# Optimization experiments

Measured on AMD Instinct MI355X. Metric: run time of the kernel, lower is better.

## Reference

```python
import jax, jax.numpy as jnp
import numpy as np

NUM_CLASSES = 2
THRESH = 0.5        # overlap_thresh
NEGPOS = 3          # neg:pos ratio
VAR = (0.1, 0.2)    # cfg['variance']
B, P, O = 64, 32768, 50


def point_form(p):
    # center-size [cx,cy,w,h] -> corner [xmin,ymin,xmax,ymax]
    return jnp.concatenate([p[:, :2] - p[:, 2:] * 0.5, p[:, :2] + p[:, 2:] * 0.5], axis=1)


def iou(a, b):
    # a [O,4], b [P,4] corner form -> [O,P]
    lt = jnp.maximum(a[:, None, :2], b[None, :, :2])
    rb = jnp.minimum(a[:, None, 2:], b[None, :, 2:])
    wh = jnp.clip(rb - lt, 0.0, None)
    inter = wh[..., 0] * wh[..., 1]
    area_a = ((a[:, 2] - a[:, 0]) * (a[:, 3] - a[:, 1]))[:, None]
    area_b = ((b[:, 2] - b[:, 0]) * (b[:, 3] - b[:, 1]))[None, :]
    return inter / (area_a + area_b - inter)


def encode(matched, priors_cs):
    g_cxcy = ((matched[:, :2] + matched[:, 2:]) * 0.5 - priors_cs[:, :2]) / (VAR[0] * priors_cs[:, 2:])
    g_wh = jnp.log((matched[:, 2:] - matched[:, :2]) / priors_cs[:, 2:]) / VAR[1]
    return jnp.concatenate([g_cxcy, g_wh], axis=1)


def match_one(truths, labels, priors_cs, priors_pt):
    ovl = iou(truths, priors_pt)                # [O,P]
    best_prior_idx = jnp.argmax(ovl, axis=1)    # [O] best prior per GT
    best_truth_ovl = jnp.max(ovl, axis=0)       # [P]
    best_truth_idx = jnp.argmax(ovl, axis=0)    # [P]
    best_truth_ovl = best_truth_ovl.at[best_prior_idx].set(2.0)
    best_truth_idx = best_truth_idx.at[best_prior_idx].set(jnp.arange(truths.shape[0]))
    matched = truths[best_truth_idx]            # [P,4]
    conf = jnp.where(best_truth_ovl < THRESH, 0, labels[best_truth_idx])
    return encode(matched, priors_cs), conf


def reference(arm_loc, arm_conf, odm_loc, odm_conf, priors, targets):
    loc_data, conf_data = arm_loc, arm_conf    # use_ARM=False -> ARM branch
    num, num_priors = loc_data.shape[0], loc_data.shape[1]
    truths = targets[..., :4]
    labels = (targets[..., 4] >= 0).astype(jnp.int32)   # num_classes == 2 binarization
    priors_pt = point_form(priors)
    loc_t, conf_t = jax.vmap(lambda t, l: match_one(t, l, priors, priors_pt))(truths, labels)
    loc_t = jax.lax.stop_gradient(loc_t)
    conf_t = jax.lax.stop_gradient(conf_t)
    pos = conf_t > 0                             # [B,P]
    # localization: smooth L1, summed over positives
    d = loc_data - loc_t
    ad = jnp.abs(d)
    sl1 = jnp.where(ad < 1.0, 0.5 * d * d, ad - 0.5)
    loss_l = jnp.sum(sl1 * pos[..., None].astype(loc_data.dtype))
    # per-prior conf loss for hard negative mining
    lse = jax.nn.logsumexp(conf_data, axis=-1)   # [B,P]
    picked = jnp.take_along_axis(conf_data, conf_t[..., None], axis=-1)[..., 0]
    lc = lse - picked                            # NLL per prior
    lc_mine = jnp.where(pos, 0.0, lc)            # zero positives before ranking
    order = jnp.argsort(-lc_mine, axis=1)        # descending sort
    rank = jnp.argsort(order, axis=1)            # rank of each prior
    num_pos = jnp.sum(pos, axis=1, keepdims=True)            # [B,1]
    num_neg = jnp.minimum(NEGPOS * num_pos, num_priors - 1)
    neg = rank < num_neg
    sel = (pos | neg).astype(conf_data.dtype)
    loss_c = jnp.sum(lc * sel)
    N = jnp.sum(num_pos).astype(loc_data.dtype)
    return loss_l / N, loss_c / N


def setup_inputs():
    key = jax.random.key(0)
    ks = jax.random.split(key, 8)
    arm_loc = jax.random.normal(ks[0], (B, P, 4), jnp.float32)
    arm_conf = jax.random.normal(ks[1], (B, P, NUM_CLASSES), jnp.float32)
    odm_loc = jax.random.normal(ks[2], (B, P, 4), jnp.float32)
    odm_conf = jax.random.normal(ks[3], (B, P, NUM_CLASSES), jnp.float32)
    # priors in center-size form
    p_cxcy = jax.random.uniform(ks[4], (P, 2), jnp.float32, 0.05, 0.95)
    p_wh = jax.random.uniform(ks[5], (P, 2), jnp.float32, 0.05, 0.5)
    priors = jnp.concatenate([p_cxcy, p_wh], axis=1)
    # GT boxes in corner form with valid extents, labels >= 0
    t_cxcy = jax.random.uniform(ks[6], (B, O, 2), jnp.float32, 0.2, 0.8)
    t_wh = jax.random.uniform(ks[7], (B, O, 2), jnp.float32, 0.05, 0.3)
    boxes = jnp.concatenate([t_cxcy - t_wh * 0.5, t_cxcy + t_wh * 0.5], axis=-1)
    targets = jnp.concatenate([boxes, jnp.ones((B, O, 1), jnp.float32)], axis=-1)
    return {"arm_loc": arm_loc, "arm_conf": arm_conf, "odm_loc": odm_loc,
            "odm_conf": odm_conf, "priors": priors, "targets": targets}
```

## Files before the change

kernel.cpp:

```cpp
#include <hip/hip_runtime.h>
#include <cstdint>

#pragma clang fp contract(off)

#define BB 64
#define PP 32768
#define OO 50
#define THRESH_F 0.5f
#define VAR0 0.1f
#define VAR1 0.2f
#define NEGPOS_I 3
#define SS 32
#define T1 4
#define NB0 2048
#define NB12 1024
#define NCELL 1024

typedef unsigned long long u64;

__device__ __forceinline__ unsigned mpart4(unsigned x) {
    x = (x | (x << 2)) & 0x33u;
    x = (x | (x << 1)) & 0x55u;
    return x;
}
__device__ __forceinline__ int cell_of(float4 pr) {
    int xb = (int)(pr.x * 16.0f); xb = xb < 0 ? 0 : (xb > 15 ? 15 : xb);
    int yb = (int)(pr.y * 16.0f); yb = yb < 0 ? 0 : (yb > 15 ? 15 : yb);
    float s = fmaxf(pr.z, pr.w);
    int wc = s < 0.275f ? 0 : (s < 0.368f ? 1 : (s < 0.44f ? 2 : 3));
    return wc * 256 + (int)(mpart4((unsigned)xb) | (mpart4((unsigned)yb) << 1));
}

__global__ void k_zero(float4* __restrict__ dst, int n4) {
    int i = blockIdx.x * blockDim.x + threadIdx.x;
    if (i < n4) dst[i] = make_float4(0.f, 0.f, 0.f, 0.f);
}

__global__ void k_phist(const float4* __restrict__ pri, int* __restrict__ cnt) {
    int p = blockIdx.x * 1024 + threadIdx.x * 4;
    for (int j = 0; j < 4; ++j)
        atomicAdd(&cnt[cell_of(pri[p + j])], 1);
}

__global__ void k_pscan(const int* __restrict__ cnt, int* __restrict__ base) {
    __shared__ int sc[256];
    int tid = threadIdx.x;
    int a[4]; int s = 0;
    for (int i = 0; i < 4; ++i) { a[i] = cnt[tid * 4 + i]; s += a[i]; }
    sc[tid] = s; __syncthreads();
    for (int off = 1; off < 256; off <<= 1) {
        int v = (tid >= off) ? sc[tid - off] : 0;
        __syncthreads(); sc[tid] += v; __syncthreads();
    }
    int excl = sc[tid] - s;
    for (int i = 0; i < 4; ++i) { base[tid * 4 + i] = excl; excl += a[i]; }
}

__global__ void k_pscat(const float4* __restrict__ pri, const int* __restrict__ base,
                        int* __restrict__ cursor, int* __restrict__ perm) {
    int p = blockIdx.x * 1024 + threadIdx.x * 4;
    for (int j = 0; j < 4; ++j) {
        int c = cell_of(pri[p + j]);
        int pos = base[c] + atomicAdd(&cursor[c], 1);
        perm[pos] = p + j;
    }
}

#define DPP_MAX(x, ctrl, rmask)                                              \
    {                                                                        \
        int _o = __float_as_int(x);                                          \
        x = fmaxf(x, __int_as_float(__builtin_amdgcn_update_dpp(             \
                _o, _o, (ctrl), (rmask), 0xf, false)));                      \
    }
#define DPP_MINI(x, ctrl, rmask)                                             \
    {                                                                        \
        int _o = (x);                                                        \
        int _s = __builtin_amdgcn_update_dpp(_o, _o, (ctrl), (rmask), 0xf, false); \
        x = (_s < x) ? _s : x;                                               \
    }

__device__ __forceinline__ float sl1enc(const float* __restrict__ tb,
                                        float4 pr, float4 ld) {
    float gx = ((tb[0] + tb[2]) * 0.5f - pr.x) / (VAR0 * pr.z);
    float gy = ((tb[1] + tb[3]) * 0.5f - pr.y) / (VAR0 * pr.w);
    float gw = logf((tb[2] - tb[0]) / pr.z) / VAR1;
    float gh = logf((tb[3] - tb[1]) / pr.w) / VAR1;
    float g[4] = {gx, gy, gw, gh};
    float l[4] = {ld.x, ld.y, ld.z, ld.w};
    float s = 0.f;
    for (int q = 0; q < 4; ++q) {
        float d = l[q] - g[q];
        float ad = fabsf(d);
        s += (ad < 1.0f) ? 0.5f * d * d : ad - 0.5f;
    }
    return s;
}

__global__ void __launch_bounds__(256, 8)
k_ml(const float* __restrict__ priors, const int* __restrict__ perm,
     const float* __restrict__ targets,
     const float* __restrict__ arm_loc, const float* __restrict__ arm_conf,
     float* __restrict__ lcm, unsigned char* __restrict__ bpi,
     u64* __restrict__ bpm,
     float* __restrict__ pll, float* __restrict__ pplc, int* __restrict__ pnp,
     int* __restrict__ Hc0, float* __restrict__ Hs0) {
    __shared__ float tr4[OO * 4];
    __shared__ float trA[OO];
    __shared__ int   trL[OO];
    __shared__ int   hc[NB0];
    __shared__ float hs[NB0];
    int b = (blockIdx.x % 8) * 8 + (blockIdx.y % 8);
    int s = (blockIdx.x / 8) + 4 * (blockIdx.y / 8);
    int tid = threadIdx.x;
    for (int i = tid; i < OO * 4; i += 256)
        tr4[i] = targets[(size_t)(b * OO + (i >> 2)) * 5 + (i & 3)];
    if (tid < OO)
        trL[tid] = (targets[(size_t)(b * OO + tid) * 5 + 4] >= 0.0f) ? 1 : 0;
    for (int i = tid; i < NB0; i += 256) { hc[i] = 0; hs[i] = 0.f; }
    __syncthreads();
    if (tid < OO)
        trA[tid] = (tr4[tid*4+2] - tr4[tid*4]) * (tr4[tid*4+3] - tr4[tid*4+1]);
    __syncthreads();

    int p0 = s * (256 * T1) + tid * T1;
    int4 o4 = ((const int4*)perm)[p0 >> 2];
    int o_[T1] = {o4.x, o4.y, o4.z, o4.w};
    int omin = min(min(o_[0], o_[1]), min(o_[2], o_[3]));
    float bx0[T1], by0[T1], bx1[T1], by1[T1], aB[T1];
#pragma unroll
    for (int j = 0; j < T1; ++j) {
        float4 pr = ((const float4*)priors)[o_[j]];
        bx0[j] = pr.x - pr.z * 0.5f; by0[j] = pr.y - pr.w * 0.5f;
        bx1[j] = pr.x + pr.z * 0.5f; by1[j] = pr.y + pr.w * 0.5f;
        aB[j] = (bx1[j] - bx0[j]) * (by1[j] - by0[j]);
    }
    float rbv[T1]; int rbi[T1];
#pragma unroll
    for (int j = 0; j < T1; ++j) { rbv[j] = 0.0f; rbi[j] = 0; }

    for (int t = 0; t < OO; ++t) {
        float t0 = tr4[t*4], t1v = tr4[t*4+1], t2 = tr4[t*4+2], t3 = tr4[t*4+3];
        float aA = trA[t];
        float I[T1];
#pragma unroll
        for (int j = 0; j < T1; ++j) {
            float ltx = fmaxf(t0, bx0[j]), lty = fmaxf(t1v, by0[j]);
            float rbx = fminf(t2, bx1[j]), rby = fminf(t3, by1[j]);
            float wx = fmaxf(rbx - ltx, 0.f), wy = fmaxf(rby - lty, 0.f);
            I[j] = wx * wy;
        }
        bool anyl = (I[0] > 0.f) | (I[1] > 0.f) | (I[2] > 0.f) | (I[3] > 0.f);
        if (__any(anyl)) {
            float cbv = 0.0f; int cbo = omin;
#pragma unroll
            for (int j = 0; j < T1; ++j) {
                float v = I[j] / (aA + aB[j] - I[j]);
                if (v > rbv[j]) { rbv[j] = v; rbi[j] = t; }
                if (v > cbv || (v == cbv && o_[j] < cbo)) { cbv = v; cbo = o_[j]; }
            }
            float x = cbv;
            DPP_MAX(x, 0x111, 0xf);
            DPP_MAX(x, 0x112, 0xf);
            DPP_MAX(x, 0x114, 0xf);
            DPP_MAX(x, 0x118, 0xf);
            DPP_MAX(x, 0x142, 0xa);
            DPP_MAX(x, 0x143, 0xc);
            float mvf = __int_as_float(__builtin_amdgcn_readlane(__float_as_int(x), 63));
            if (mvf > 0.0f) {
                int key = (cbv == mvf) ? cbo : 0x7FFFFFFF;
                DPP_MINI(key, 0x111, 0xf);
                DPP_MINI(key, 0x112, 0xf);
                DPP_MINI(key, 0x114, 0xf);
                DPP_MINI(key, 0x118, 0xf);
                DPP_MINI(key, 0x142, 0xa);
                DPP_MINI(key, 0x143, 0xc);
                int morig = __builtin_amdgcn_readlane(key, 63);
                if ((tid & 63) == 0) {
                    u64 pk = ((u64)__float_as_uint(mvf) << 32) | (unsigned)(PP - morig);
                    atomicMax(&bpm[b * OO + t], pk);
                }
            }
        }
    }

    size_t bbase = (size_t)b * PP;
    float ll = 0.0f, plc = 0.0f; int np = 0;
#pragma unroll
    for (int c = 0; c < T1; ++c) {
        int o = o_[c]; size_t bo = bbase + o;
        int ti = rbi[c]; float ov = rbv[c];
        int conf = (ov < THRESH_F) ? 0 : trL[ti];
        float2 cf = ((const float2*)arm_conf)[bo];
        float c0 = cf.x, c1 = cf.y;
        float m = fmaxf(c0, c1);
        float lse = logf(expf(c0 - m) + expf(c1 - m)) + m;
        bool pos = conf > 0;
        float lc = lse - (pos ? c1 : c0);
        float outv = pos ? 0.0f : lc;
        lcm[bo] = outv;
        bpi[bo] = (unsigned char)((pos ? 0x80u : 0u) | (unsigned)ti);
        unsigned u = __float_as_uint(outv);
        atomicAdd(&hc[u >> 20], 1);
        atomicAdd(&hs[u >> 20], outv);
        if (pos) {
            np++; plc += lc;
            float4 pr = ((const float4*)priors)[o];
            float4 ld = ((const float4*)arm_loc)[bo];
            ll += sl1enc(&tr4[ti * 4], pr, ld);
        }
    }

    __syncthreads();
    for (int i = tid; i < NB0; i += 256) {
        int cv = hc[i];
        if (cv) {
            atomicAdd(&Hc0[b * NB0 + i], cv);
            atomicAdd(&Hs0[b * NB0 + i], hs[i]);
        }
    }
    __syncthreads();
    float* s1 = (float*)hc;
    int*   s3 = hc + 256;
    float* s2 = hs;
    s1[tid] = ll; s2[tid] = plc; s3[tid] = np;
    __syncthreads();
    for (int st = 128; st > 0; st >>= 1) {
        if (tid < st) { s1[tid] += s1[tid+st]; s2[tid] += s2[tid+st]; s3[tid] += s3[tid+st]; }
        __syncthreads();
    }
    if (tid == 0) {
        pll[s * BB + b] = s1[0];
        pplc[s * BB + b] = s2[0];
        pnp[s * BB + b] = s3[0];
    }
}

__global__ void k_fix(const u64* __restrict__ bpm, const float* __restrict__ targets,
                      const float* __restrict__ arm_loc, const float* __restrict__ arm_conf,
                      const float* __restrict__ priors, const unsigned char* __restrict__ bpi,
                      float* __restrict__ lcm,
                      float* __restrict__ pll, float* __restrict__ pplc,
                      int* __restrict__ pnp, int* __restrict__ npb,
                      int* __restrict__ Hc0, float* __restrict__ Hs0) {
    int b = blockIdx.x, j = threadIdx.x;
    int p = -1;
    if (j < OO) {
        unsigned lo = (unsigned)(bpm[b * OO + j] & 0xFFFFFFFFull);
        p = lo ? (PP - (int)lo) : 0;
    }
    bool w = (j < OO);
    for (int jj = 1; jj < OO; ++jj) {
        int pj = __shfl(p, jj, 64);
        if (jj > j && pj == p) w = false;
    }
    float dll = 0.f, dplc = 0.f; int dnp = 0;
    if (w) {
        size_t bp = (size_t)b * PP + p;
        unsigned char ob = bpi[bp];
        bool old_pos = (ob & 0x80u) != 0;
        int old_ti = ob & 63;
        float2 cf = ((const float2*)arm_conf)[bp];
        float c0 = cf.x, c1 = cf.y;
        float m = fmaxf(c0, c1);
        float lse = logf(expf(c0 - m) + expf(c1 - m)) + m;
        const float* tbj = &targets[(size_t)(b * OO + j) * 5];
        bool new_pos = (tbj[4] >= 0.0f);
        float old_lcm = lcm[bp];
        float new_lcm = new_pos ? 0.0f : (lse - c0);
        unsigned uo = __float_as_uint(old_lcm), un = __float_as_uint(new_lcm);
        if (uo != un) {
            atomicAdd(&Hc0[b * NB0 + (uo >> 20)], -1);
            atomicAdd(&Hs0[b * NB0 + (uo >> 20)], -old_lcm);
            atomicAdd(&Hc0[b * NB0 + (un >> 20)], 1);
            atomicAdd(&Hs0[b * NB0 + (un >> 20)], new_lcm);
            lcm[bp] = new_lcm;
        }
        float4 pr = ((const float4*)priors)[p];
        float4 ld = ((const float4*)arm_loc)[bp];
        if (old_pos) {
            dnp -= 1; dplc -= (lse - c1);
            dll -= sl1enc(&targets[(size_t)(b * OO + old_ti) * 5], pr, ld);
        }
        if (new_pos) {
            dnp += 1; dplc += (lse - c1);
            dll += sl1enc(tbj, pr, ld);
        }
    }
    int myp = (j < SS) ? pnp[j * BB + b] : 0;
    for (int s = 32; s >= 1; s >>= 1) {
        dll += __shfl_down(dll, s, 64);
        dplc += __shfl_down(dplc, s, 64);
        dnp += __shfl_down(dnp, s, 64);
        myp += __shfl_down(myp, s, 64);
    }
    if (j == 0) {
        pll[b] += dll;
        pplc[b] += dplc;
        pnp[b] += dnp;
        npb[b] = myp + dnp;
    }
}

__global__ void __launch_bounds__(256)
k_sel(const float* __restrict__ lcm, const int* __restrict__ npb,
      int* __restrict__ Hc0, float* __restrict__ Hs0,
      float* __restrict__ ssum, int* __restrict__ srem, unsigned* __restrict__ stb) {
    __shared__ int hc[NB12]; __shared__ float hs[NB12];
    __shared__ int sc[256]; __shared__ float sf[256];
    __shared__ int s_chunk, s_r; __shared__ float s_S; __shared__ unsigned s_pref;
    int b = blockIdx.x, tid = threadIdx.x;

    {
        const int* hcg = Hc0 + b * NB0; const float* hsg = Hs0 + b * NB0;
        int c = 0; float f = 0.f; int base = tid * 8;
        for (int i = 0; i < 8; ++i) { c += hcg[base + i]; f += hsg[base + i]; }
        sc[tid] = c; sf[tid] = f;
        if (tid == 0) {
            int k = NEGPOS_I * npb[b]; if (k > PP - 1) k = PP - 1;
            s_r = k; s_S = 0.f;
        }
        __syncthreads();
        for (int off = 1; off < 256; off <<= 1) {
            int cv = (tid + off < 256) ? sc[tid + off] : 0;
            float fv = (tid + off < 256) ? sf[tid + off] : 0.f;
            __syncthreads(); sc[tid] += cv; sf[tid] += fv; __syncthreads();
        }
        int r = s_r;
        int nxt = (tid == 255) ? 0 : sc[tid + 1];
        if (sc[tid] >= r && nxt < r) s_chunk = tid;
        __syncthreads();
        if (tid == 0) {
            int ch = s_chunk;
            int r2 = r - ((ch == 255) ? 0 : sc[ch + 1]);
            float S2 = s_S + ((ch == 255) ? 0.f : sf[ch + 1]);
            int binSel = ch * 8;
            for (int i = 7; i >= 0; --i) {
                int bin = ch * 8 + i; int cbn = hcg[bin];
                if (r2 <= cbn) { binSel = bin; break; }
                r2 -= cbn; S2 += hsg[bin];
            }
            s_pref = (unsigned)binSel; s_r = r2; s_S = S2;
        }
        __syncthreads();
    }
    {
        for (int i = tid; i < NB12; i += 256) { hc[i] = 0; hs[i] = 0.f; }
        __syncthreads();
        unsigned pref = s_pref;
        const float4* v4 = (const float4*)(lcm + (size_t)b * PP);
        for (int it = 0; it < 32; ++it) {
            float4 x = v4[it * 256 + tid];
            float xs[4] = {x.x, x.y, x.z, x.w};
            for (int c2 = 0; c2 < 4; ++c2) {
                unsigned u = __float_as_uint(xs[c2]);
                if ((u >> 20) == pref) {
                    atomicAdd(&hc[(u >> 10) & 1023u], 1);
                    atomicAdd(&hs[(u >> 10) & 1023u], xs[c2]);
                }
            }
        }
        __syncthreads();
        int c = 0; float f = 0.f; int base = tid * 4;
        for (int i = 0; i < 4; ++i) { c += hc[base + i]; f += hs[base + i]; }
        sc[tid] = c; sf[tid] = f; __syncthreads();
        for (int off = 1; off < 256; off <<= 1) {
            int cv = (tid + off < 256) ? sc[tid + off] : 0;
            float fv = (tid + off < 256) ? sf[tid + off] : 0.f;
            __syncthreads(); sc[tid] += cv; sf[tid] += fv; __syncthreads();
        }
        int r = s_r;
        int nxt = (tid == 255) ? 0 : sc[tid + 1];
        if (sc[tid] >= r && nxt < r) s_chunk = tid;
        __syncthreads();
        if (tid == 0) {
            int ch = s_chunk;
            int r2 = r - ((ch == 255) ? 0 : sc[ch + 1]);
            float S2 = s_S + ((ch == 255) ? 0.f : sf[ch + 1]);
            int binSel = ch * 4;
            for (int i = 3; i >= 0; --i) {
                int bin = ch * 4 + i; int cbn = hc[bin];
                if (r2 <= cbn) { binSel = bin; break; }
                r2 -= cbn; S2 += hs[bin];
            }
            s_pref = (s_pref << 10) | (unsigned)binSel; s_r = r2; s_S = S2;
        }
        __syncthreads();
    }
    {
        for (int i = tid; i < NB12; i += 256) { hc[i] = 0; hs[i] = 0.f; }
        __syncthreads();
        unsigned pref = s_pref;
        const float4* v4 = (const float4*)(lcm + (size_t)b * PP);
        for (int it = 0; it < 32; ++it) {
            float4 x = v4[it * 256 + tid];
            float xs[4] = {x.x, x.y, x.z, x.w};
            for (int c2 = 0; c2 < 4; ++c2) {
                unsigned u = __float_as_uint(xs[c2]);
                if ((u >> 10) == pref) {
                    atomicAdd(&hc[u & 1023u], 1);
                    atomicAdd(&hs[u & 1023u], xs[c2]);
                }
            }
        }
        __syncthreads();
        int c = 0; float f = 0.f; int base = tid * 4;
        for (int i = 0; i < 4; ++i) { c += hc[base + i]; f += hs[base + i]; }
        sc[tid] = c; sf[tid] = f; __syncthreads();
        for (int off = 1; off < 256; off <<= 1) {
            int cv = (tid + off < 256) ? sc[tid + off] : 0;
            float fv = (tid + off < 256) ? sf[tid + off] : 0.f;
            __syncthreads(); sc[tid] += cv; sf[tid] += fv; __syncthreads();
        }
        int r = s_r;
        int nxt = (tid == 255) ? 0 : sc[tid + 1];
        if (sc[tid] >= r && nxt < r) s_chunk = tid;
        __syncthreads();
        if (tid == 0) {
            int ch = s_chunk;
            int r2 = r - ((ch == 255) ? 0 : sc[ch + 1]);
            float S2 = s_S + ((ch == 255) ? 0.f : sf[ch + 1]);
            int binSel = ch * 4;
            for (int i = 3; i >= 0; --i) {
                int bin = ch * 4 + i; int cbn = hc[bin];
                if (r2 <= cbn) { binSel = bin; break; }
                r2 -= cbn; S2 += hs[bin];
            }
            stb[b] = (s_pref << 10) | (unsigned)binSel;
            srem[b] = r2; ssum[b] = S2;
        }
    }
}

__global__ void k_final(const float* __restrict__ pll, const float* __restrict__ pplc,
                        const int* __restrict__ pnp, const float* __restrict__ ssum,
                        const int* __restrict__ srem, const unsigned* __restrict__ stb,
                        float* __restrict__ out) {
    int b = threadIdx.x;
    float ll = 0.f, plc = 0.f; int np = 0;
    for (int s = 0; s < SS; ++s) {
        ll += pll[s * BB + b];
        plc += pplc[s * BB + b];
        np += pnp[s * BB + b];
    }
    float tval = __uint_as_float(stb[b]);
    float cc = plc + ssum[b] + (float)srem[b] * tval;
    for (int s = 32; s > 0; s >>= 1) {
        ll += __shfl_down(ll, s);
        cc += __shfl_down(cc, s);
        np += __shfl_down(np, s);
    }
    if (b == 0) {
        float N = (float)np;
        out[0] = ll / N;
        out[1] = cc / N;
    }
}

extern "C" void kernel_launch(void* const* d_in, const int* in_sizes, int n_in,
                              void* d_out, int out_size, void* d_ws, size_t ws_size,
                              hipStream_t stream) {
    const float* arm_loc  = (const float*)d_in[0];
    const float* arm_conf = (const float*)d_in[1];
    const float* priors   = (const float*)d_in[4];
    const float* targets  = (const float*)d_in[5];
    float* out = (float*)d_out;

    char* w = (char*)d_ws;
    float* lcm = (float*)w;  w += sizeof(float) * (size_t)BB * PP;
    unsigned char* bpi = (unsigned char*)w; w += (size_t)BB * PP;
    char* zbase = w;
    int*   Hc0 = (int*)w;    w += sizeof(int)   * BB * NB0;
    float* Hs0 = (float*)w;  w += sizeof(float) * BB * NB0;
    u64*   bpm = (u64*)w;    w += sizeof(u64)   * BB * OO;
    int*   cellCnt = (int*)w; w += sizeof(int) * NCELL;
    int*   cursor  = (int*)w; w += sizeof(int) * NCELL;
    size_t zbytes = (size_t)(w - zbase);
    int*   cellBase = (int*)w; w += sizeof(int) * NCELL;
    int*   perm = (int*)w;   w += sizeof(int) * PP;
    float* pll  = (float*)w; w += sizeof(float) * BB * SS;
    float* pplc = (float*)w; w += sizeof(float) * BB * SS;
    int*   pnp  = (int*)w;   w += sizeof(int)   * BB * SS;
    int*   npb  = (int*)w;   w += sizeof(int)   * BB;
    int*      srem = (int*)w;      w += sizeof(int) * BB;
    float*    ssum = (float*)w;    w += sizeof(float) * BB;
    unsigned* stb  = (unsigned*)w; w += sizeof(unsigned) * BB;

    int n4 = (int)(zbytes / 16);
    k_zero<<<(n4 + 255) / 256, 256, 0, stream>>>((float4*)zbase, n4);
    k_phist<<<PP / 1024, 256, 0, stream>>>((const float4*)priors, cellCnt);
    k_pscan<<<1, 256, 0, stream>>>(cellCnt, cellBase);
    k_pscat<<<PP / 1024, 256, 0, stream>>>((const float4*)priors, cellBase, cursor, perm);
    k_ml<<<dim3(SS, BB), 256, 0, stream>>>(priors, perm, targets, arm_loc, arm_conf,
                                           lcm, bpi, bpm, pll, pplc, pnp, Hc0, Hs0);
    k_fix<<<BB, 64, 0, stream>>>(bpm, targets, arm_loc, arm_conf, priors, bpi,
                                 lcm, pll, pplc, pnp, npb, Hc0, Hs0);
    k_sel<<<BB, 256, 0, stream>>>(lcm, npb, Hc0, Hs0, ssum, srem, stb);
    k_final<<<1, 64, 0, stream>>>(pll, pplc, pnp, ssum, srem, stb, out);
}
```

Measured before the change: 280.5 us.

## Fuse prefix kernels, cull targets per wave, store permuted loss, merge tail kernels

Merges the prior cell scan and scatter into one kernel, with each block redoing the small scan, and adds an inverse permutation. In the matching loop, each wave computes a bounding box of its priors and skips ground-truth boxes that cannot overlap it. Per-prior loss values and match bytes are now stored in sorted (permuted) order as vectorised writes instead of scattered ones, and the fix, selection and final reduction kernels are combined into one tail kernel that finishes with a global atomic counter. Together these cut kernel launches and scattered stores, at the cost of extra atomics and an iperm lookup in the fix step.

```diff
diff --git a/kernel.cpp b/kernel.cpp
--- a/kernel.cpp
+++ b/kernel.cpp
@@ -42,8 +42,11 @@
         atomicAdd(&cnt[cell_of(pri[p + j])], 1);
 }
 
-__global__ void k_pscan(const int* __restrict__ cnt, int* __restrict__ base) {
+__global__ void __launch_bounds__(256)
+k_pss(const float4* __restrict__ pri, const int* __restrict__ cnt,
+      int* __restrict__ cursor, int* __restrict__ perm, int* __restrict__ iperm) {
     __shared__ int sc[256];
+    __shared__ int sbase[NCELL];
     int tid = threadIdx.x;
     int a[4]; int s = 0;
     for (int i = 0; i < 4; ++i) { a[i] = cnt[tid * 4 + i]; s += a[i]; }
@@ -53,16 +56,14 @@
         __syncthreads(); sc[tid] += v; __syncthreads();
     }
     int excl = sc[tid] - s;
-    for (int i = 0; i < 4; ++i) { base[tid * 4 + i] = excl; excl += a[i]; }
-}
-
-__global__ void k_pscat(const float4* __restrict__ pri, const int* __restrict__ base,
-                        int* __restrict__ cursor, int* __restrict__ perm) {
-    int p = blockIdx.x * 1024 + threadIdx.x * 4;
+    for (int i = 0; i < 4; ++i) { sbase[tid * 4 + i] = excl; excl += a[i]; }
+    __syncthreads();
+    int p = blockIdx.x * 1024 + tid * 4;
     for (int j = 0; j < 4; ++j) {
         int c = cell_of(pri[p + j]);
-        int pos = base[c] + atomicAdd(&cursor[c], 1);
+        int pos = sbase[c] + atomicAdd(&cursor[c], 1);
         perm[pos] = p + j;
+        iperm[p + j] = pos;
     }
 }
 
@@ -72,12 +73,24 @@
         x = fmaxf(x, __int_as_float(__builtin_amdgcn_update_dpp(             \
                 _o, _o, (ctrl), (rmask), 0xf, false)));                      \
     }
+#define DPP_MINF(x, ctrl, rmask)                                             \
+    {                                                                        \
+        int _o = __float_as_int(x);                                          \
+        x = fminf(x, __int_as_float(__builtin_amdgcn_update_dpp(             \
+                _o, _o, (ctrl), (rmask), 0xf, false)));                      \
+    }
 #define DPP_MINI(x, ctrl, rmask)                                             \
     {                                                                        \
         int _o = (x);                                                        \
         int _s = __builtin_amdgcn_update_dpp(_o, _o, (ctrl), (rmask), 0xf, false); \
         x = (_s < x) ? _s : x;                                               \
     }
+#define WAVE_MAXF(x) { DPP_MAX(x,0x111,0xf); DPP_MAX(x,0x112,0xf); DPP_MAX(x,0x114,0xf); \
+                       DPP_MAX(x,0x118,0xf); DPP_MAX(x,0x142,0xa); DPP_MAX(x,0x143,0xc); }
+#define WAVE_MINF(x) { DPP_MINF(x,0x111,0xf); DPP_MINF(x,0x112,0xf); DPP_MINF(x,0x114,0xf); \
+                       DPP_MINF(x,0x118,0xf); DPP_MINF(x,0x142,0xa); DPP_MINF(x,0x143,0xc); }
+#define WAVE_MINI(x) { DPP_MINI(x,0x111,0xf); DPP_MINI(x,0x112,0xf); DPP_MINI(x,0x114,0xf); \
+                       DPP_MINI(x,0x118,0xf); DPP_MINI(x,0x142,0xa); DPP_MINI(x,0x143,0xc); }
 
 __device__ __forceinline__ float sl1enc(const float* __restrict__ tb,
                                         float4 pr, float4 ld) {
@@ -100,26 +113,24 @@
 k_ml(const float* __restrict__ priors, const int* __restrict__ perm,
      const float* __restrict__ targets,
      const float* __restrict__ arm_loc, const float* __restrict__ arm_conf,
-     float* __restrict__ lcm, unsigned char* __restrict__ bpi,
+     float* __restrict__ lcmP, unsigned char* __restrict__ bpiP,
      u64* __restrict__ bpm,
      float* __restrict__ pll, float* __restrict__ pplc, int* __restrict__ pnp,
      int* __restrict__ Hc0, float* __restrict__ Hs0) {
-    __shared__ float tr4[OO * 4];
-    __shared__ float trA[OO];
-    __shared__ int   trL[OO];
+    __shared__ float4 trP[OO];
+    __shared__ float2 trQ[OO];
     __shared__ int   hc[NB0];
     __shared__ float hs[NB0];
     int b = (blockIdx.x % 8) * 8 + (blockIdx.y % 8);
     int s = (blockIdx.x / 8) + 4 * (blockIdx.y / 8);
     int tid = threadIdx.x;
-    for (int i = tid; i < OO * 4; i += 256)
-        tr4[i] = targets[(size_t)(b * OO + (i >> 2)) * 5 + (i & 3)];
-    if (tid < OO)
-        trL[tid] = (targets[(size_t)(b * OO + tid) * 5 + 4] >= 0.0f) ? 1 : 0;
+    if (tid < OO) {
+        const float* tb = &targets[(size_t)(b * OO + tid) * 5];
+        float x0 = tb[0], y0 = tb[1], x1 = tb[2], y1 = tb[3];
+        trP[tid] = make_float4(x0, y0, x1, y1);
+        trQ[tid] = make_float2((x1 - x0) * (y1 - y0), tb[4]);
+    }
     for (int i = tid; i < NB0; i += 256) { hc[i] = 0; hs[i] = 0.f; }
-    __syncthreads();
-    if (tid < OO)
-        trA[tid] = (tr4[tid*4+2] - tr4[tid*4]) * (tr4[tid*4+3] - tr4[tid*4+1]);
     __syncthreads();
 
     int p0 = s * (256 * T1) + tid * T1;
@@ -134,18 +145,29 @@
         bx1[j] = pr.x + pr.z * 0.5f; by1[j] = pr.y + pr.w * 0.5f;
         aB[j] = (bx1[j] - bx0[j]) * (by1[j] - by0[j]);
     }
+    float lx0 = fminf(fminf(bx0[0], bx0[1]), fminf(bx0[2], bx0[3]));
+    float ly0 = fminf(fminf(by0[0], by0[1]), fminf(by0[2], by0[3]));
+    float lx1 = fmaxf(fmaxf(bx1[0], bx1[1]), fmaxf(bx1[2], bx1[3]));
+    float ly1 = fmaxf(fmaxf(by1[0], by1[1]), fmaxf(by1[2], by1[3]));
+    WAVE_MINF(lx0); WAVE_MINF(ly0); WAVE_MAXF(lx1); WAVE_MAXF(ly1);
+    float wx0 = __int_as_float(__builtin_amdgcn_readlane(__float_as_int(lx0), 63));
+    float wy0 = __int_as_float(__builtin_amdgcn_readlane(__float_as_int(ly0), 63));
+    float wx1 = __int_as_float(__builtin_amdgcn_readlane(__float_as_int(lx1), 63));
+    float wy1 = __int_as_float(__builtin_amdgcn_readlane(__float_as_int(ly1), 63));
+
     float rbv[T1]; int rbi[T1];
 #pragma unroll
     for (int j = 0; j < T1; ++j) { rbv[j] = 0.0f; rbi[j] = 0; }
 
     for (int t = 0; t < OO; ++t) {
-        float t0 = tr4[t*4], t1v = tr4[t*4+1], t2 = tr4[t*4+2], t3 = tr4[t*4+3];
-        float aA = trA[t];
+        float4 tP = trP[t];
+        if (!(tP.z > wx0 && tP.x < wx1 && tP.w > wy0 && tP.y < wy1)) continue;
+        float aA = trQ[t].x;
         float I[T1];
 #pragma unroll
         for (int j = 0; j < T1; ++j) {
-            float ltx = fmaxf(t0, bx0[j]), lty = fmaxf(t1v, by0[j]);
-            float rbx = fminf(t2, bx1[j]), rby = fminf(t3, by1[j]);
+            float ltx = fmaxf(tP.x, bx0[j]), lty = fmaxf(tP.y, by0[j]);
+            float rbx = fminf(tP.z, bx1[j]), rby = fminf(tP.w, by1[j]);
             float wx = fmaxf(rbx - ltx, 0.f), wy = fmaxf(rby - lty, 0.f);
             I[j] = wx * wy;
         }
@@ -159,21 +181,11 @@
                 if (v > cbv || (v == cbv && o_[j] < cbo)) { cbv = v; cbo = o_[j]; }
             }
             float x = cbv;
-            DPP_MAX(x, 0x111, 0xf);
-            DPP_MAX(x, 0x112, 0xf);
-            DPP_MAX(x, 0x114, 0xf);
-            DPP_MAX(x, 0x118, 0xf);
-            DPP_MAX(x, 0x142, 0xa);
-            DPP_MAX(x, 0x143, 0xc);
+            WAVE_MAXF(x);
             float mvf = __int_as_float(__builtin_amdgcn_readlane(__float_as_int(x), 63));
             if (mvf > 0.0f) {
                 int key = (cbv == mvf) ? cbo : 0x7FFFFFFF;
-                DPP_MINI(key, 0x111, 0xf);
-                DPP_MINI(key, 0x112, 0xf);
-                DPP_MINI(key, 0x114, 0xf);
-                DPP_MINI(key, 0x118, 0xf);
-                DPP_MINI(key, 0x142, 0xa);
-                DPP_MINI(key, 0x143, 0xc);
+                WAVE_MINI(key);
                 int morig = __builtin_amdgcn_readlane(key, 63);
                 if ((tid & 63) == 0) {
                     u64 pk = ((u64)__float_as_uint(mvf) << 32) | (unsigned)(PP - morig);
@@ -185,30 +197,34 @@
 
     size_t bbase = (size_t)b * PP;
     float ll = 0.0f, plc = 0.0f; int np = 0;
+    float outv[4]; unsigned pbyte = 0;
 #pragma unroll
     for (int c = 0; c < T1; ++c) {
         int o = o_[c]; size_t bo = bbase + o;
         int ti = rbi[c]; float ov = rbv[c];
-        int conf = (ov < THRESH_F) ? 0 : trL[ti];
         float2 cf = ((const float2*)arm_conf)[bo];
         float c0 = cf.x, c1 = cf.y;
         float m = fmaxf(c0, c1);
         float lse = logf(expf(c0 - m) + expf(c1 - m)) + m;
-        bool pos = conf > 0;
+        bool pos = (ov >= THRESH_F) && (trQ[ti].y >= 0.0f);
         float lc = lse - (pos ? c1 : c0);
-        float outv = pos ? 0.0f : lc;
-        lcm[bo] = outv;
-        bpi[bo] = (unsigned char)((pos ? 0x80u : 0u) | (unsigned)ti);
-        unsigned u = __float_as_uint(outv);
+        outv[c] = pos ? 0.0f : lc;
+        pbyte |= (unsigned)((pos ? 0x80u : 0u) | (unsigned)ti) << (8 * c);
+        unsigned u = __float_as_uint(outv[c]);
         atomicAdd(&hc[u >> 20], 1);
-        atomicAdd(&hs[u >> 20], outv);
+        atomicAdd(&hs[u >> 20], outv[c]);
         if (pos) {
             np++; plc += lc;
             float4 pr = ((const float4*)priors)[o];
             float4 ld = ((const float4*)arm_loc)[bo];
-            ll += sl1enc(&tr4[ti * 4], pr, ld);
-        }
-    }
+            const float4 tv = trP[ti];
+            float tb4[4] = {tv.x, tv.y, tv.z, tv.w};
+            ll += sl1enc(tb4, pr, ld);
+        }
+    }
+    size_t bq = bbase + p0;
+    ((float4*)lcmP)[bq >> 2] = make_float4(outv[0], outv[1], outv[2], outv[3]);
+    ((unsigned*)bpiP)[bq >> 2] = pbyte;
 
     __syncthreads();
     for (int i = tid; i < NB0; i += 256) {
@@ -235,80 +251,83 @@
     }
 }
 
-__global__ void k_fix(const u64* __restrict__ bpm, const float* __restrict__ targets,
-                      const float* __restrict__ arm_loc, const float* __restrict__ arm_conf,
-                      const float* __restrict__ priors, const unsigned char* __restrict__ bpi,
-                      float* __restrict__ lcm,
-                      float* __restrict__ pll, float* __restrict__ pplc,
-                      int* __restrict__ pnp, int* __restrict__ npb,
-                      int* __restrict__ Hc0, float* __restrict__ Hs0) {
-    int b = blockIdx.x, j = threadIdx.x;
-    int p = -1;
-    if (j < OO) {
-        unsigned lo = (unsigned)(bpm[b * OO + j] & 0xFFFFFFFFull);
-        p = lo ? (PP - (int)lo) : 0;
-    }
-    bool w = (j < OO);
-    for (int jj = 1; jj < OO; ++jj) {
-        int pj = __shfl(p, jj, 64);
-        if (jj > j && pj == p) w = false;
-    }
-    float dll = 0.f, dplc = 0.f; int dnp = 0;
-    if (w) {
-        size_t bp = (size_t)b * PP + p;
-        unsigned char ob = bpi[bp];
-        bool old_pos = (ob & 0x80u) != 0;
-        int old_ti = ob & 63;
-        float2 cf = ((const float2*)arm_conf)[bp];
-        float c0 = cf.x, c1 = cf.y;
-        float m = fmaxf(c0, c1);
-        float lse = logf(expf(c0 - m) + expf(c1 - m)) + m;
-        const float* tbj = &targets[(size_t)(b * OO + j) * 5];
-        bool new_pos = (tbj[4] >= 0.0f);
-        float old_lcm = lcm[bp];
-        float new_lcm = new_pos ? 0.0f : (lse - c0);
-        unsigned uo = __float_as_uint(old_lcm), un = __float_as_uint(new_lcm);
-        if (uo != un) {
-            atomicAdd(&Hc0[b * NB0 + (uo >> 20)], -1);
-            atomicAdd(&Hs0[b * NB0 + (uo >> 20)], -old_lcm);
-            atomicAdd(&Hc0[b * NB0 + (un >> 20)], 1);
-            atomicAdd(&Hs0[b * NB0 + (un >> 20)], new_lcm);
-            lcm[bp] = new_lcm;
-        }
-        float4 pr = ((const float4*)priors)[p];
-        float4 ld = ((const float4*)arm_loc)[bp];
-        if (old_pos) {
-            dnp -= 1; dplc -= (lse - c1);
-            dll -= sl1enc(&targets[(size_t)(b * OO + old_ti) * 5], pr, ld);
-        }
-        if (new_pos) {
-            dnp += 1; dplc += (lse - c1);
-            dll += sl1enc(tbj, pr, ld);
-        }
-    }
-    int myp = (j < SS) ? pnp[j * BB + b] : 0;
-    for (int s = 32; s >= 1; s >>= 1) {
-        dll += __shfl_down(dll, s, 64);
-        dplc += __shfl_down(dplc, s, 64);
-        dnp += __shfl_down(dnp, s, 64);
-        myp += __shfl_down(myp, s, 64);
-    }
-    if (j == 0) {
-        pll[b] += dll;
-        pplc[b] += dplc;
-        pnp[b] += dnp;
-        npb[b] = myp + dnp;
-    }
-}
-
 __global__ void __launch_bounds__(256)
-k_sel(const float* __restrict__ lcm, const int* __restrict__ npb,
-      int* __restrict__ Hc0, float* __restrict__ Hs0,
-      float* __restrict__ ssum, int* __restrict__ srem, unsigned* __restrict__ stb) {
+k_tail(const u64* __restrict__ bpm, const float* __restrict__ targets,
+       const float* __restrict__ arm_loc, const float* __restrict__ arm_conf,
+       const float* __restrict__ priors, const int* __restrict__ iperm,
+       float* __restrict__ lcmP, const unsigned char* __restrict__ bpiP,
+       const float* __restrict__ pll, const float* __restrict__ pplc,
+       const int* __restrict__ pnp,
+       int* __restrict__ Hc0, float* __restrict__ Hs0,
+       float* __restrict__ gacc, int* __restrict__ gcnt,
+       float* __restrict__ out) {
     __shared__ int hc[NB12]; __shared__ float hs[NB12];
     __shared__ int sc[256]; __shared__ float sf[256];
     __shared__ int s_chunk, s_r; __shared__ float s_S; __shared__ unsigned s_pref;
+    __shared__ float s_llb, s_plcb; __shared__ int s_npb;
     int b = blockIdx.x, tid = threadIdx.x;
+    size_t bbase = (size_t)b * PP;
+
+    if (tid < 64) {
+        int j = tid;
+        int p = -1;
+        if (j < OO) {
+            unsigned lo = (unsigned)(bpm[b * OO + j] & 0xFFFFFFFFull);
+            p = lo ? (PP - (int)lo) : 0;
+        }
+        bool w = (j < OO);
+        for (int jj = 1; jj < OO; ++jj) {
+            int pj = __shfl(p, jj, 64);
+            if (jj > j && pj == p) w = false;
+        }
+        float dll = 0.f, dplc = 0.f; int dnp = 0;
+        if (w) {
+            int pos = iperm[p];
+            size_t bq = bbase + pos;
+            size_t bo = bbase + p;
+            unsigned char ob = bpiP[bq];
+            bool old_pos = (ob & 0x80u) != 0;
+            int old_ti = ob & 63;
+            float2 cf = ((const float2*)arm_conf)[bo];
+            float c0 = cf.x, c1 = cf.y;
+            float m = fmaxf(c0, c1);
+            float lse = logf(expf(c0 - m) + expf(c1 - m)) + m;
+            const float* tbj = &targets[(size_t)(b * OO + j) * 5];
+            bool new_pos = (tbj[4] >= 0.0f);
+            float old_lcm = lcmP[bq];
+            float new_lcm = new_pos ? 0.0f : (lse - c0);
+            unsigned uo = __float_as_uint(old_lcm), un = __float_as_uint(new_lcm);
+            if (uo != un) {
+                atomicAdd(&Hc0[b * NB0 + (uo >> 20)], -1);
+                atomicAdd(&Hs0[b * NB0 + (uo >> 20)], -old_lcm);
+                atomicAdd(&Hc0[b * NB0 + (un >> 20)], 1);
+                atomicAdd(&Hs0[b * NB0 + (un >> 20)], new_lcm);
+                atomicExch(&lcmP[bq], new_lcm);
+            }
+            float4 pr = ((const float4*)priors)[p];
+            float4 ld = ((const float4*)arm_loc)[bo];
+            if (old_pos) {
+                dnp -= 1; dplc -= (lse - c1);
+                dll -= sl1enc(&targets[(size_t)(b * OO + old_ti) * 5], pr, ld);
+            }
+            if (new_pos) {
+                dnp += 1; dplc += (lse - c1);
+                dll += sl1enc(tbj, pr, ld);
+            }
+        }
+        float myll = (j < SS) ? pll[j * BB + b] : 0.f;
+        float mypl = (j < SS) ? pplc[j * BB + b] : 0.f;
+        int   mynp = (j < SS) ? pnp[j * BB + b] : 0;
+        dll += myll; dplc += mypl; dnp += mynp;
+        for (int st = 32; st >= 1; st >>= 1) {
+            dll += __shfl_down(dll, st, 64);
+            dplc += __shfl_down(dplc, st, 64);
+            dnp += __shfl_down(dnp, st, 64);
+        }
+        if (j == 0) { s_llb = dll; s_plcb = dplc; s_npb = dnp; }
+    }
+    __threadfence();
+    __syncthreads();
 
     {
         const int* hcg = Hc0 + b * NB0; const float* hsg = Hs0 + b * NB0;
@@ -316,7 +335,7 @@
         for (int i = 0; i < 8; ++i) { c += hcg[base + i]; f += hsg[base + i]; }
         sc[tid] = c; sf[tid] = f;
         if (tid == 0) {
-            int k = NEGPOS_I * npb[b]; if (k > PP - 1) k = PP - 1;
+            int k = NEGPOS_I * s_npb; if (k > PP - 1) k = PP - 1;
             s_r = k; s_S = 0.f;
         }
         __syncthreads();
@@ -347,7 +366,7 @@
         for (int i = tid; i < NB12; i += 256) { hc[i] = 0; hs[i] = 0.f; }
         __syncthreads();
         unsigned pref = s_pref;
-        const float4* v4 = (const float4*)(lcm + (size_t)b * PP);
+        const float4* v4 = (const float4*)(lcmP + bbase);
         for (int it = 0; it < 32; ++it) {
             float4 x = v4[it * 256 + tid];
             float xs[4] = {x.x, x.y, x.z, x.w};
@@ -390,7 +409,7 @@
         for (int i = tid; i < NB12; i += 256) { hc[i] = 0; hs[i] = 0.f; }
         __syncthreads();
         unsigned pref = s_pref;
-        const float4* v4 = (const float4*)(lcm + (size_t)b * PP);
+        const float4* v4 = (const float4*)(lcmP + bbase);
         for (int it = 0; it < 32; ++it) {
             float4 x = v4[it * 256 + tid];
             float xs[4] = {x.x, x.y, x.z, x.w};
@@ -425,34 +444,21 @@
                 if (r2 <= cbn) { binSel = bin; break; }
                 r2 -= cbn; S2 += hs[bin];
             }
-            stb[b] = (s_pref << 10) | (unsigned)binSel;
-            srem[b] = r2; ssum[b] = S2;
-        }
-    }
-}
-
-__global__ void k_final(const float* __restrict__ pll, const float* __restrict__ pplc,
-                        const int* __restrict__ pnp, const float* __restrict__ ssum,
-                        const int* __restrict__ srem, const unsigned* __restrict__ stb,
-                        float* __restrict__ out) {
-    int b = threadIdx.x;
-    float ll = 0.f, plc = 0.f; int np = 0;
-    for (int s = 0; s < SS; ++s) {
-        ll += pll[s * BB + b];
-        plc += pplc[s * BB + b];
-        np += pnp[s * BB + b];
-    }
-    float tval = __uint_as_float(stb[b]);
-    float cc = plc + ssum[b] + (float)srem[b] * tval;
-    for (int s = 32; s > 0; s >>= 1) {
-        ll += __shfl_down(ll, s);
-        cc += __shfl_down(cc, s);
-        np += __shfl_down(np, s);
-    }
-    if (b == 0) {
-        float N = (float)np;
-        out[0] = ll / N;
-        out[1] = cc / N;
+            unsigned tb = (s_pref << 10) | (unsigned)binSel;
+            float tval = __uint_as_float(tb);
+            float ccb = s_plcb + S2 + (float)r2 * tval;
+            float llb = s_llb; int npb = s_npb;
+            float oll = atomicAdd(&gacc[0], llb);
+            float occ = atomicAdd(&gacc[1], ccb);
+            int onp = atomicAdd(&gcnt[0], npb);
+            __threadfence();
+            int tk = atomicAdd(&gcnt[1], 1);
+            if (tk == BB - 1) {
+                float N = (float)(onp + npb);
+                out[0] = (oll + llb) / N;
+                out[1] = (occ + ccb) / N;
+            }
+        }
     }
 }
 
@@ -466,34 +472,29 @@
     float* out = (float*)d_out;
 
     char* w = (char*)d_ws;
-    float* lcm = (float*)w;  w += sizeof(float) * (size_t)BB * PP;
-    unsigned char* bpi = (unsigned char*)w; w += (size_t)BB * PP;
+    float* lcmP = (float*)w;  w += sizeof(float) * (size_t)BB * PP;
+    unsigned char* bpiP = (unsigned char*)w; w += (size_t)BB * PP;
     char* zbase = w;
     int*   Hc0 = (int*)w;    w += sizeof(int)   * BB * NB0;
     float* Hs0 = (float*)w;  w += sizeof(float) * BB * NB0;
     u64*   bpm = (u64*)w;    w += sizeof(u64)   * BB * OO;
     int*   cellCnt = (int*)w; w += sizeof(int) * NCELL;
     int*   cursor  = (int*)w; w += sizeof(int) * NCELL;
+    float* gacc = (float*)w;  w += sizeof(float) * 2;
+    int*   gcnt = (int*)w;    w += sizeof(int) * 2;
     size_t zbytes = (size_t)(w - zbase);
-    int*   cellBase = (int*)w; w += sizeof(int) * NCELL;
-    int*   perm = (int*)w;   w += sizeof(int) * PP;
+    int*   perm  = (int*)w;  w += sizeof(int) * PP;
+    int*   iperm = (int*)w;  w += sizeof(int) * PP;
     float* pll  = (float*)w; w += sizeof(float) * BB * SS;
     float* pplc = (float*)w; w += sizeof(float) * BB * SS;
     int*   pnp  = (int*)w;   w += sizeof(int)   * BB * SS;
-    int*   npb  = (int*)w;   w += sizeof(int)   * BB;
-    int*      srem = (int*)w;      w += sizeof(int) * BB;
-    float*    ssum = (float*)w;    w += sizeof(float) * BB;
-    unsigned* stb  = (unsigned*)w; w += sizeof(unsigned) * BB;
 
     int n4 = (int)(zbytes / 16);
     k_zero<<<(n4 + 255) / 256, 256, 0, stream>>>((float4*)zbase, n4);
     k_phist<<<PP / 1024, 256, 0, stream>>>((const float4*)priors, cellCnt);
-    k_pscan<<<1, 256, 0, stream>>>(cellCnt, cellBase);
-    k_pscat<<<PP / 1024, 256, 0, stream>>>((const float4*)priors, cellBase, cursor, perm);
+    k_pss<<<PP / 1024, 256, 0, stream>>>((const float4*)priors, cellCnt, cursor, perm, iperm);
     k_ml<<<dim3(SS, BB), 256, 0, stream>>>(priors, perm, targets, arm_loc, arm_conf,
-                                           lcm, bpi, bpm, pll, pplc, pnp, Hc0, Hs0);
-    k_fix<<<BB, 64, 0, stream>>>(bpm, targets, arm_loc, arm_conf, priors, bpi,
-                                 lcm, pll, pplc, pnp, npb, Hc0, Hs0);
-    k_sel<<<BB, 256, 0, stream>>>(lcm, npb, Hc0, Hs0, ssum, srem, stb);
-    k_final<<<1, 64, 0, stream>>>(pll, pplc, pnp, ssum, srem, stb, out);
-}
+                                           lcmP, bpiP, bpm, pll, pplc, pnp, Hc0, Hs0);
+    k_tail<<<BB, 256, 0, stream>>>(bpm, targets, arm_loc, arm_conf, priors, iperm,
+                                   lcmP, bpiP, pll, pplc, pnp, Hc0, Hs0, gacc, gcnt, out);
+}
```

Result: faster. 274.8 us (-2.0%).
